# Kernel optimization log

Measured on AMD Instinct MI355X. Metric: run time of the kernel, lower is better.

The kernel has to match this reference:

```python
import jax, jax.numpy as jnp
import numpy as np


def spline_conv(x, src, dst, u, Wk, Wroot, bias, num_nodes):
    # Linear B-spline basis for dim=1, kernel_size=2, degree=1: [(1-u), u]
    # Transform at node level first (cheap GEMM), then gather/blend per edge.
    h0 = x @ Wk[0]           # [N, out]
    h1 = x @ Wk[1]           # [N, out]
    w1 = u[:, 0]             # [E]
    w0 = 1.0 - w1
    msg = w0[:, None] * h0[src] + w1[:, None] * h1[src]   # [E, out]
    agg = jax.ops.segment_sum(msg, dst, num_segments=num_nodes)
    deg = jax.ops.segment_sum(jnp.ones_like(w1), dst, num_segments=num_nodes)
    agg = agg / jnp.maximum(deg, 1.0)[:, None]             # aggr='mean'
    return agg + x @ Wroot + bias


def setup_inputs() -> dict:
    key = jax.random.key(0)
    k = jax.random.split(key, 10)
    N, F_IN, HID, C, E = 100000, 128, 16, 10, 1600000
    x = jax.random.normal(k[0], (N, F_IN), dtype=jnp.float32)
    edge_index = jax.random.randint(k[1], (2, E), 0, N, dtype=jnp.int64)
    edge_attr = jax.random.uniform(k[2], (E, 1), dtype=jnp.float32)
    s1 = 1.0 / np.sqrt(F_IN)
    s2 = 1.0 / np.sqrt(HID)
    W1 = jax.random.uniform(k[3], (2, F_IN, HID), jnp.float32, -s1, s1)
    root1 = jax.random.uniform(k[4], (F_IN, HID), jnp.float32, -s1, s1)
    b1 = jax.random.uniform(k[5], (HID,), jnp.float32, -s1, s1)
    W2 = jax.random.uniform(k[6], (2, HID, C), jnp.float32, -s2, s2)
    root2 = jax.random.uniform(k[7], (HID, C), jnp.float32, -s2, s2)
    b2 = jax.random.uniform(k[8], (C,), jnp.float32, -s2, s2)
    return {"x": x, "edge_index": edge_index, "edge_attr": edge_attr,
            "W1": W1, "root1": root1, "b1": b1,
            "W2": W2, "root2": root2, "b2": b2}


def reference(x, edge_index, edge_attr, W1, root1, b1, W2, root2, b2):
    N = x.shape[0]
    src, dst = edge_index[0], edge_index[1]
    # dropout is identity in eval mode
    h = spline_conv(x, src, dst, edge_attr, W1, root1, b1, N)
    h = jax.nn.elu(h)
    out = spline_conv(h, src, dst, edge_attr, W2, root2, b2, N)
    return out
```

## Files before the change

kernel.cpp:

```cpp
#include <hip/hip_runtime.h>
#include <math.h>


#define SHIFT    7
#define BNODES   128
#define NBUK_MAX 800
#define CAP      2432
#define CHUNK    4096

__device__ __forceinline__ unsigned short f2bf(float f) {
    unsigned int u = __float_as_uint(f);
    u += 0x7FFF + ((u >> 16) & 1);
    return (unsigned short)(u >> 16);
}


__device__ __forceinline__ void gemm_part(
    float* __restrict__ Ws, int gb, int tid,
    const float* __restrict__ x, const float* __restrict__ W1,
    const float* __restrict__ root1, unsigned int* __restrict__ h01i,
    float* __restrict__ xr, int N)
{
    for (int idx = tid; idx < 128 * 48; idx += 256) {
        int k = idx / 48, j = idx % 48;
        int grp = j >> 3, t = j & 7;
        float v;
        switch (grp) {
            case 0: v = W1[k * 16 + t];            break;
            case 1: v = W1[2048 + k * 16 + t];     break;
            case 2: v = root1[k * 16 + t];         break;
            case 3: v = W1[k * 16 + 8 + t];        break;
            case 4: v = W1[2048 + k * 16 + 8 + t]; break;
            default: v = root1[k * 16 + 8 + t];    break;
        }
        Ws[idx] = v;
    }
    __syncthreads();
    int nl   = tid >> 1;
    int half = tid & 1;
    int n = gb * 128 + nl;
    if (n >= N) return;

    float acc[24];
#pragma unroll
    for (int j = 0; j < 24; ++j) acc[j] = 0.f;

    const float4* xrow = (const float4*)(x + (size_t)n * 128);
    const float4* wbase = (const float4*)(Ws + half * 24);
#pragma unroll 8
    for (int k4 = 0; k4 < 32; ++k4) {
        float4 xv = xrow[k4];
        float xs[4] = {xv.x, xv.y, xv.z, xv.w};
#pragma unroll
        for (int kk = 0; kk < 4; ++kk) {
            float xk = xs[kk];
            const float4* w4 = wbase + ((k4 * 4 + kk) * 48) / 4;
#pragma unroll
            for (int q = 0; q < 6; ++q) {
                float4 wv = w4[q];
                acc[q * 4 + 0] += xk * wv.x;
                acc[q * 4 + 1] += xk * wv.y;
                acc[q * 4 + 2] += xk * wv.z;
                acc[q * 4 + 3] += xk * wv.w;
            }
        }
    }
    int cb = half * 8;
#pragma unroll
    for (int t = 0; t < 8; ++t)
        h01i[(size_t)n * 16 + cb + t] =
            (unsigned int)f2bf(acc[t]) | ((unsigned int)f2bf(acc[8 + t]) << 16);
#pragma unroll
    for (int t = 0; t < 8; ++t)
        xr[(size_t)n * 16 + cb + t] = acc[16 + t];
}

__device__ __forceinline__ void bin_part(
    int* __restrict__ smem, int bb, int tid,
    const int* __restrict__ ei, const float* __restrict__ ea,
    int* __restrict__ gcur, int2* __restrict__ staging, int E, int nbuk)
{
    int* bcnt  = smem;
    int* gbase = bcnt + NBUK_MAX;
    for (int i = tid; i < nbuk; i += 256) bcnt[i] = 0;
    __syncthreads();

    int base = bb * CHUNK;
    int lrank[16];
#pragma unroll
    for (int i = 0; i < 16; ++i) {
        int e = base + i * 256 + tid;
        lrank[i] = 0;
        if (e < E) lrank[i] = atomicAdd(&bcnt[ei[E + e] >> SHIFT], 1);
    }
    __syncthreads();
    for (int b = tid; b < nbuk; b += 256) {
        int c = bcnt[b];
        gbase[b] = c ? atomicAdd(&gcur[b], c) : 0;
    }
    __syncthreads();
#pragma unroll
    for (int i = 0; i < 16; ++i) {
        int e = base + i * 256 + tid;
        if (e < E) {
            int s = ei[e];
            int d = ei[E + e];
            int b = d >> SHIFT;
            int p = gbase[b] + lrank[i];
            if (p < CAP)
                staging[(size_t)b * CAP + p] =
                    make_int2(s | ((d & (BNODES - 1)) << 17), __float_as_int(ea[e]));
        }
    }
}

__global__ __launch_bounds__(256, 4) void phase1_kernel(
    const float* __restrict__ x, const float* __restrict__ W1,
    const float* __restrict__ root1, unsigned int* __restrict__ h01i,
    float* __restrict__ xr,
    const int* __restrict__ ei, const float* __restrict__ ea,
    int* __restrict__ gcur, int2* __restrict__ staging,
    int N, int E, int nbuk, int gemmBlocks, int binBlocks)
{
    __shared__ float smem[128 * 48];
    int tid = threadIdx.x;
    int bid = blockIdx.x;
    int sub = bid >> 1;
    if ((bid & 1) == 0) {
        if (sub < gemmBlocks)
            gemm_part(smem, sub, tid, x, W1, root1, h01i, xr, N);
    } else {
        if (sub < binBlocks)
            bin_part((int*)smem, sub, tid, ei, ea, gcur, staging, E, nbuk);
    }
}

__global__ __launch_bounds__(256) void csr_build_kernel(
    int2* __restrict__ staging, const int* __restrict__ gcur,
    int* __restrict__ roff, int* __restrict__ cnt, int N)
{
    __shared__ int2 rin[CAP];
    __shared__ unsigned int rout[CAP];
    __shared__ int hist[BNODES];
    __shared__ int sscan[BNODES];
    __shared__ int wcur[BNODES];
    int tid = threadIdx.x;
    int b = blockIdx.x;
    int m = gcur[b];
    if (m > CAP) m = CAP;
    int2* sp = staging + (size_t)b * CAP;

    if (tid < BNODES) { hist[tid] = 0; wcur[tid] = 0; }
    __syncthreads();
    for (int k = tid; k < m; k += 256) {
        int2 r = sp[k];
        rin[k] = r;
        atomicAdd(&hist[r.x >> 17], 1);
    }
    __syncthreads();
    if (tid < BNODES) sscan[tid] = hist[tid];
    __syncthreads();
    for (int off = 1; off < BNODES; off <<= 1) {
        int t = (tid < BNODES && tid >= off) ? sscan[tid - off] : 0;
        __syncthreads();
        if (tid < BNODES) sscan[tid] += t;
        __syncthreads();
    }
    for (int k = tid; k < m; k += 256) {
        int2 r = rin[k];
        int dl = r.x >> 17;
        int pos = (sscan[dl] - hist[dl]) + atomicAdd(&wcur[dl], 1);
        float w = __int_as_float(r.y);
        int wq = (int)(w * 32768.0f + 0.5f);
        if (wq > 32767) wq = 32767;
        rout[pos] = (unsigned int)(r.x & 0x1FFFF) | ((unsigned int)wq << 17);
    }
    __syncthreads();
    unsigned int* sp32 = (unsigned int*)sp;
    for (int k = tid; k < m; k += 256) sp32[k] = rout[k];
    if (tid < BNODES) {
        int n = b * BNODES + tid;
        if (n < N) {
            roff[n] = b * (CAP * 2) + (sscan[tid] - hist[tid]);
            cnt[n]  = hist[tid];
        }
    }
}

__global__ __launch_bounds__(256) void gather1f_kernel(
    const unsigned int* __restrict__ staging, const int* __restrict__ roff,
    const int* __restrict__ cnt, const unsigned int* __restrict__ h01i,
    const float* __restrict__ xr, const float* __restrict__ b1,
    const float* __restrict__ root2, const float* __restrict__ b2,
    unsigned short* __restrict__ hb, float* __restrict__ hrb, int N)
{
    __shared__ float r2s[160];
    __shared__ float b1s[16];
    __shared__ float b2s[10];
    int tid = threadIdx.x;
    if (tid < 160) r2s[tid] = root2[tid];
    if (tid < 16)  b1s[tid] = b1[tid];
    if (tid < 10)  b2s[tid] = b2[tid];
    __syncthreads();
    int t = blockIdx.x * 256 + tid;
    int n = t >> 4;
    int c = t & 15;
    if (n >= N) return;
    int start = roff[n];
    int m = cnt[n];
    float acc = 0.f;
#pragma unroll 4
    for (int k = 0; k < m; ++k) {
        unsigned int rec = staging[(size_t)start + k];
        float w = (float)(rec >> 17) * (1.0f / 32768.0f);
        unsigned int v = h01i[(size_t)(rec & 0x1FFFF) * 16 + c];
        float a  = __uint_as_float(v << 16);
        float bb = __uint_as_float(v & 0xFFFF0000u);
        acc += a + w * (bb - a);
    }
    float invd = 1.0f / fmaxf((float)m, 1.0f);
    float hv = acc * invd + xr[(size_t)n * 16 + c] + b1s[c];
    hv = hv > 0.f ? hv : expm1f(hv);
    hb[(size_t)n * 16 + c] = f2bf(hv);

    float r[10];
#pragma unroll
    for (int j = 0; j < 10; ++j) r[j] = hv * r2s[c * 10 + j];
#pragma unroll
    for (int off = 1; off < 16; off <<= 1) {
#pragma unroll
        for (int j = 0; j < 10; ++j) r[j] += __shfl_xor(r[j], off);
    }
    if (c == 0) {
        float* hp = hrb + (size_t)n * 10;
#pragma unroll
        for (int j = 0; j < 10; ++j) hp[j] = r[j] + b2s[j];
    }
}

__global__ __launch_bounds__(256) void gather2f_kernel(
    const unsigned int* __restrict__ staging, const int* __restrict__ roff,
    const int* __restrict__ cnt, const unsigned short* __restrict__ hb,
    const float* __restrict__ hrb, const float* __restrict__ W2,
    float* __restrict__ out, int N)
{
    __shared__ float w2s[320];
    int tid = threadIdx.x;
    for (int idx = tid; idx < 320; idx += 256) w2s[idx] = W2[idx];
    __syncthreads();
    int t = blockIdx.x * 256 + tid;
    int n = t >> 4;
    int c = t & 15;
    if (n >= N) return;
    int start = roff[n];
    int m = cnt[n];
    float p = 0.f, q = 0.f;
#pragma unroll 4
    for (int k = 0; k < m; ++k) {
        unsigned int rec = staging[(size_t)start + k];
        float w = (float)(rec >> 17) * (1.0f / 32768.0f);
        float v = __uint_as_float(((unsigned int)hb[(size_t)(rec & 0x1FFFF) * 16 + c]) << 16);
        p += (1.f - w) * v;
        q += w * v;
    }
    float invd = 1.0f / fmaxf((float)m, 1.0f);
    float o[10];
#pragma unroll
    for (int j = 0; j < 10; ++j)
        o[j] = p * w2s[c * 10 + j] + q * w2s[160 + c * 10 + j];
#pragma unroll
    for (int off = 1; off < 16; off <<= 1) {
#pragma unroll
        for (int j = 0; j < 10; ++j) o[j] += __shfl_xor(o[j], off);
    }
    if (c == 0) {
        float* op = out + (size_t)n * 10;
        const float* hp = hrb + (size_t)n * 10;
#pragma unroll
        for (int j = 0; j < 10; ++j) op[j] = o[j] * invd + hp[j];
    }
}

extern "C" void kernel_launch(void* const* d_in, const int* in_sizes, int n_in,
                              void* d_out, int out_size, void* d_ws, size_t ws_size,
                              hipStream_t stream)
{
    const float* x     = (const float*)d_in[0];
    const int*   ei    = (const int*)d_in[1];
    const float* ea    = (const float*)d_in[2];
    const float* W1    = (const float*)d_in[3];
    const float* root1 = (const float*)d_in[4];
    const float* b1    = (const float*)d_in[5];
    const float* W2    = (const float*)d_in[6];
    const float* root2 = (const float*)d_in[7];
    const float* b2    = (const float*)d_in[8];
    float* out = (float*)d_out;

    int N = in_sizes[0] / 128;
    int E = in_sizes[2];
    int nbuk = (N + BNODES - 1) / BNODES;

    char* ws = (char*)d_ws;
    int2*  staging = (int2*)ws;
    unsigned int* h01i = (unsigned int*)(ws + (size_t)nbuk * CAP * 8);
    float* xr    = (float*)(h01i + (size_t)N * 16);
    float* hrb   = xr + (size_t)N * 16;
    unsigned short* hb = (unsigned short*)(hrb + (size_t)N * 10);
    int*   cnt   = (int*)(hb + (size_t)N * 16);
    int*   roff  = cnt + N;
    int*   gcur  = roff + N;

    int nb_e16 = (N * 16 + 255) / 256;
    int gemmBlocks = (N + 127) / 128;
    int binBlocks  = (E + CHUNK - 1) / CHUNK;
    int mixBlocks  = 2 * ((gemmBlocks > binBlocks) ? gemmBlocks : binBlocks);

    hipMemsetAsync(gcur, 0, (size_t)nbuk * sizeof(int), stream);

    phase1_kernel   <<<mixBlocks, 256, 0, stream>>>(
        x, W1, root1, h01i, xr, ei, ea, gcur, staging, N, E, nbuk,
        gemmBlocks, binBlocks);
    csr_build_kernel<<<nbuk, 256, 0, stream>>>(staging, gcur, roff, cnt, N);
    gather1f_kernel <<<nb_e16, 256, 0, stream>>>((const unsigned int*)staging,
                                                 roff, cnt, h01i, xr,
                                                 b1, root2, b2, hb, hrb, N);
    gather2f_kernel <<<nb_e16, 256, 0, stream>>>((const unsigned int*)staging,
                                                 roff, cnt, hb, hrb,
                                                 W2, out, N);
}
```

Measured before the change: 134.8 us.

## Pack edge staging records into 32-bit words and enlarge binning chunks

Each staged edge record shrinks from an int2 (packed src/dst-local plus float weight) to one 32-bit word holding the source index, an 8-bit quantized weight and the 7-bit local destination. This halves staging writes and reads and removes the weight quantization from the CSR build pass. The binning chunk grows fourfold, so there are fewer bin blocks and fewer global atomics on the bucket counters. Per-edge ranks now come from a second shared-memory atomic pass instead of being held in registers. In exchange, edge weights keep only 8 bits of precision instead of 15, which risks accuracy, and each bin block does more serial work.

```diff
diff --git a/kernel.cpp b/kernel.cpp
--- a/kernel.cpp
+++ b/kernel.cpp
@@ -6,7 +6,8 @@
 #define BNODES   128
 #define NBUK_MAX 800
 #define CAP      2432
-#define CHUNK    4096
+#define CHUNK    16384
+#define BITER    (CHUNK / 256)
 
 __device__ __forceinline__ unsigned short f2bf(float f) {
     unsigned int u = __float_as_uint(f);
@@ -78,20 +79,19 @@
 __device__ __forceinline__ void bin_part(
     int* __restrict__ smem, int bb, int tid,
     const int* __restrict__ ei, const float* __restrict__ ea,
-    int* __restrict__ gcur, int2* __restrict__ staging, int E, int nbuk)
+    int* __restrict__ gcur, unsigned int* __restrict__ staging, int E, int nbuk)
 {
     int* bcnt  = smem;
     int* gbase = bcnt + NBUK_MAX;
-    for (int i = tid; i < nbuk; i += 256) bcnt[i] = 0;
+    int* wcur  = gbase + NBUK_MAX;
+    for (int i = tid; i < nbuk; i += 256) { bcnt[i] = 0; wcur[i] = 0; }
     __syncthreads();
 
     int base = bb * CHUNK;
-    int lrank[16];
-#pragma unroll
-    for (int i = 0; i < 16; ++i) {
+#pragma unroll 4
+    for (int i = 0; i < BITER; ++i) {
         int e = base + i * 256 + tid;
-        lrank[i] = 0;
-        if (e < E) lrank[i] = atomicAdd(&bcnt[ei[E + e] >> SHIFT], 1);
+        if (e < E) atomicAdd(&bcnt[ei[E + e] >> SHIFT], 1);
     }
     __syncthreads();
     for (int b = tid; b < nbuk; b += 256) {
@@ -99,17 +99,20 @@
         gbase[b] = c ? atomicAdd(&gcur[b], c) : 0;
     }
     __syncthreads();
-#pragma unroll
-    for (int i = 0; i < 16; ++i) {
+#pragma unroll 4
+    for (int i = 0; i < BITER; ++i) {
         int e = base + i * 256 + tid;
         if (e < E) {
             int s = ei[e];
             int d = ei[E + e];
             int b = d >> SHIFT;
-            int p = gbase[b] + lrank[i];
+            int p = gbase[b] + atomicAdd(&wcur[b], 1);
+            int wq = (int)(ea[e] * 256.0f + 0.5f);
+            if (wq > 255) wq = 255;
             if (p < CAP)
                 staging[(size_t)b * CAP + p] =
-                    make_int2(s | ((d & (BNODES - 1)) << 17), __float_as_int(ea[e]));
+                    (unsigned int)s | ((unsigned int)wq << 17)
+                                    | ((unsigned int)(d & (BNODES - 1)) << 25);
         }
     }
 }
@@ -119,7 +122,7 @@
     const float* __restrict__ root1, unsigned int* __restrict__ h01i,
     float* __restrict__ xr,
     const int* __restrict__ ei, const float* __restrict__ ea,
-    int* __restrict__ gcur, int2* __restrict__ staging,
+    int* __restrict__ gcur, unsigned int* __restrict__ staging,
     int N, int E, int nbuk, int gemmBlocks, int binBlocks)
 {
     __shared__ float smem[128 * 48];
@@ -136,10 +139,10 @@
 }
 
 __global__ __launch_bounds__(256) void csr_build_kernel(
-    int2* __restrict__ staging, const int* __restrict__ gcur,
+    unsigned int* __restrict__ staging, const int* __restrict__ gcur,
     int* __restrict__ roff, int* __restrict__ cnt, int N)
 {
-    __shared__ int2 rin[CAP];
+    __shared__ unsigned int rin[CAP];
     __shared__ unsigned int rout[CAP];
     __shared__ int hist[BNODES];
     __shared__ int sscan[BNODES];
@@ -148,14 +151,14 @@
     int b = blockIdx.x;
     int m = gcur[b];
     if (m > CAP) m = CAP;
-    int2* sp = staging + (size_t)b * CAP;
+    unsigned int* sp = staging + (size_t)b * CAP;
 
     if (tid < BNODES) { hist[tid] = 0; wcur[tid] = 0; }
     __syncthreads();
     for (int k = tid; k < m; k += 256) {
-        int2 r = sp[k];
+        unsigned int r = sp[k];
         rin[k] = r;
-        atomicAdd(&hist[r.x >> 17], 1);
+        atomicAdd(&hist[r >> 25], 1);
     }
     __syncthreads();
     if (tid < BNODES) sscan[tid] = hist[tid];
@@ -167,21 +170,17 @@
         __syncthreads();
     }
     for (int k = tid; k < m; k += 256) {
-        int2 r = rin[k];
-        int dl = r.x >> 17;
+        unsigned int r = rin[k];
+        int dl = r >> 25;
         int pos = (sscan[dl] - hist[dl]) + atomicAdd(&wcur[dl], 1);
-        float w = __int_as_float(r.y);
-        int wq = (int)(w * 32768.0f + 0.5f);
-        if (wq > 32767) wq = 32767;
-        rout[pos] = (unsigned int)(r.x & 0x1FFFF) | ((unsigned int)wq << 17);
-    }
-    __syncthreads();
-    unsigned int* sp32 = (unsigned int*)sp;
-    for (int k = tid; k < m; k += 256) sp32[k] = rout[k];
+        rout[pos] = (r & 0x1FFFF) | (((r >> 17) & 0xFF) << 24);
+    }
+    __syncthreads();
+    for (int k = tid; k < m; k += 256) sp[k] = rout[k];
     if (tid < BNODES) {
         int n = b * BNODES + tid;
         if (n < N) {
-            roff[n] = b * (CAP * 2) + (sscan[tid] - hist[tid]);
+            roff[n] = b * CAP + (sscan[tid] - hist[tid]);
             cnt[n]  = hist[tid];
         }
     }
@@ -301,8 +300,8 @@
     int nbuk = (N + BNODES - 1) / BNODES;
 
     char* ws = (char*)d_ws;
-    int2*  staging = (int2*)ws;
-    unsigned int* h01i = (unsigned int*)(ws + (size_t)nbuk * CAP * 8);
+    unsigned int* staging = (unsigned int*)ws;
+    unsigned int* h01i = (unsigned int*)(ws + (size_t)nbuk * CAP * 4);
     float* xr    = (float*)(h01i + (size_t)N * 16);
     float* hrb   = xr + (size_t)N * 16;
     unsigned short* hb = (unsigned short*)(hrb + (size_t)N * 10);
@@ -321,10 +320,8 @@
         x, W1, root1, h01i, xr, ei, ea, gcur, staging, N, E, nbuk,
         gemmBlocks, binBlocks);
     csr_build_kernel<<<nbuk, 256, 0, stream>>>(staging, gcur, roff, cnt, N);
-    gather1f_kernel <<<nb_e16, 256, 0, stream>>>((const unsigned int*)staging,
-                                                 roff, cnt, h01i, xr,
+    gather1f_kernel <<<nb_e16, 256, 0, stream>>>(staging, roff, cnt, h01i, xr,
                                                  b1, root2, b2, hb, hrb, N);
-    gather2f_kernel <<<nb_e16, 256, 0, stream>>>((const unsigned int*)staging,
-                                                 roff, cnt, hb, hrb,
+    gather2f_kernel <<<nb_e16, 256, 0, stream>>>(staging, roff, cnt, hb, hrb,
                                                  W2, out, N);
 }
```

Result: slower. 149.4 us (+10.9%).
